# Kernel optimization log

Measured on AMD Instinct MI355X. Metric: run time of the kernel, lower is better.

Reference implementation:

```python
import jax, jax.numpy as jnp
jax.config.update("jax_enable_x64", True)
import numpy as np

LEAF = 0.3          # leaf_voxel_size
FACTOR = 2.0        # scale_up_factor
LEVELS = 3          # voxel_level_num
DIM = 8             # feature_dim
BUF = 5000000       # hash_buffer_size
NFEAT = 4194304     # entries per level feature table
PRIMES = jnp.array([73856093, 19349669, 83492791], dtype=jnp.int64)
STEPS = jnp.array([[0.,0.,0.],[0.,0.,1.],[0.,1.,0.],[0.,1.,1.],
                   [1.,0.,0.],[1.,0.,1.],[1.,1.,0.],[1.,1.,1.]], dtype=jnp.float32)

def setup_inputs() -> dict:
    key = jax.random.key(0)
    k1, k2, k3 = jax.random.split(key, 3)
    query_points = jax.random.normal(k1, (1000000, 3), dtype=jnp.float32) * 25.0
    features = 0.01 * jax.random.normal(k2, (LEVELS, NFEAT, DIM), dtype=jnp.float32)
    index_table = jax.random.randint(k3, (LEVELS, BUF), 0, NFEAT, dtype=jnp.int64)
    return {"query_points": query_points, "features": features, "index_table": index_table}

def _level_features(points, feats, idx_table, res):
    # points: [N,3], feats: [F,D], idx_table: [BUF] int64
    base = jnp.floor(points / res)                       # [N,3]
    corners = base[:, None, :] + STEPS[None]             # [N,8,3]
    keys = (corners.astype(jnp.int64) * PRIMES).sum(-1) % BUF  # [N,8]
    idx = idx_table[keys]                                # [N,8]
    mask = idx.min(axis=1) > -1                          # point valid iff all 8 corners mapped
    gathered = feats[jnp.maximum(idx, 0)]                # [N,8,D]
    d = points / res - base                              # fractional coords in cell, [N,3]
    # trilinear weights, corner order matches STEPS (same as torch interpolat)
    w = (STEPS[None] * d[:, None, :] + (1.0 - STEPS[None]) * (1.0 - d[:, None, :])).prod(-1)  # [N,8]
    lvl = (gathered * w[..., None]).sum(1)               # [N,D]
    return jnp.where(mask[:, None], lvl, 0.0)

def reference(query_points, features, index_table):
    out = jnp.zeros((query_points.shape[0], DIM), dtype=jnp.float32)
    for i in range(LEVELS):
        res = LEAF * FACTOR ** i
        out = out + _level_features(query_points, features[i], index_table[i], res)
    return out
```

## Files before the change

### kernel.cpp

```cpp
#include <hip/hip_runtime.h>


constexpr int       BUF   = 5000000;
constexpr long long NFEAT = 4194304;
constexpr int       DIM   = 8;
constexpr long long P0 = 73856093, P1 = 19349669, P2 = 83492791;
constexpr int       NBINS = 1 << 21;

typedef float vf4 __attribute__((ext_vector_type(4)));

#define GLD0(dst, voff, base)                                  \
    asm volatile("global_load_dwordx4 %0, %1, %2"              \
                 : "=v"(dst) : "v"(voff), "s"(base))
#define GLD16(dst, voff, base)                                 \
    asm volatile("global_load_dwordx4 %0, %1, %2 offset:16"    \
                 : "=v"(dst) : "v"(voff), "s"(base))

template <bool ADD>
__global__ __launch_bounds__(256, 4) void nvh_level_kernel(
    const float* __restrict__ in,
    const float* __restrict__ fb,
    const int* __restrict__ tab,
    float* __restrict__ outp,
    int n, float res)
{
    int i = blockIdx.x * blockDim.x + threadIdx.x;
    if (i >= n) return;

    const float px = in[3 * i + 0];
    const float py = in[3 * i + 1];
    const float pz = in[3 * i + 2];

    const float fx = px / res, fy = py / res, fz = pz / res;
    const float bx = floorf(fx), by = floorf(fy), bz = floorf(fz);
    const float dx = fx - bx, dy = fy - by, dz = fz - bz;

    const long long ix = (long long)bx;
    const long long iy = (long long)by;
    const long long iz = (long long)bz;

    long long h0 = (ix * P0 + iy * P1 + iz * P2) % (long long)BUF;
    if (h0 < 0) h0 += BUF;
    const int k0 = (int)h0;

    int idxv[8];
#pragma unroll
    for (int c = 0; c < 8; ++c) {
        const long long offc = (((c >> 2) & 1) * P0 + ((c >> 1) & 1) * P1 +
                                (c & 1) * P2) % (long long)BUF;
        int k = k0 + (int)offc;
        if (k >= BUF) k -= BUF;
        idxv[c] = tab[k];
    }
    __builtin_amdgcn_sched_barrier(0);

    bool valid = true;
    unsigned voff[8];
#pragma unroll
    for (int c = 0; c < 8; ++c) {
        valid = valid && (idxv[c] > -1);
        const int id = idxv[c] > 0 ? idxv[c] : 0;
        voff[c] = (unsigned)id * 32u;
    }

    vf4 f[16];
#pragma unroll
    for (int c = 0; c < 8; ++c) {
        GLD0 (f[2 * c + 0], voff[c], fb);
        GLD16(f[2 * c + 1], voff[c], fb);
    }

    vf4 prev0, prev1;
    if (ADD) {
        const vf4* op = (const vf4*)(outp + (size_t)i * DIM);
        prev0 = op[0];
        prev1 = op[1];
    }

    const float wx1 = dx, wx0 = 1.0f - dx;
    const float wy1 = dy, wy0 = 1.0f - dy;
    const float wz1 = dz, wz0 = 1.0f - dz;
    const float vmask = valid ? 1.0f : 0.0f;

    asm volatile("s_waitcnt vmcnt(0)" ::: "memory");
    __builtin_amdgcn_sched_barrier(0);

    vf4 lacc0 = (vf4)0.0f;
    vf4 lacc1 = (vf4)0.0f;
#pragma unroll
    for (int c = 0; c < 8; ++c) {
        const float wc = (((c >> 2) & 1) ? wx1 : wx0) *
                         (((c >> 1) & 1) ? wy1 : wy0) *
                         (((c     ) & 1) ? wz1 : wz0);
        lacc0 += wc * f[2 * c + 0];
        lacc1 += wc * f[2 * c + 1];
    }

    vf4 r0 = vmask * lacc0;
    vf4 r1 = vmask * lacc1;
    if (ADD) { r0 += prev0; r1 += prev1; }

    vf4* op = (vf4*)(outp + (size_t)i * DIM);
    op[0] = r0;
    op[1] = r1;
}

__device__ __forceinline__ unsigned spread3(unsigned v) {
    v = (v | (v << 16)) & 0x030000FFu;
    v = (v | (v << 8))  & 0x0300F00Fu;
    v = (v | (v << 4))  & 0x030C30C3u;
    v = (v | (v << 2))  & 0x09249249u;
    return v;
}

__global__ __launch_bounds__(256) void zero_hist(unsigned* __restrict__ h) {
    int i = blockIdx.x * blockDim.x + threadIdx.x;
    for (int k = i; k < NBINS; k += gridDim.x * blockDim.x) h[k] = 0u;
}

__global__ __launch_bounds__(256) void keys_hist(
    const float* __restrict__ qp, unsigned* __restrict__ keys,
    unsigned* __restrict__ hist, int n)
{
    int i = blockIdx.x * blockDim.x + threadIdx.x;
    if (i >= n) return;
    const float inv = 1.0f / 1.2f;
    int cx = (int)floorf(qp[3 * i + 0] * inv);
    int cy = (int)floorf(qp[3 * i + 1] * inv);
    int cz = (int)floorf(qp[3 * i + 2] * inv);
    cx = cx < -64 ? -64 : (cx > 63 ? 63 : cx);
    cy = cy < -64 ? -64 : (cy > 63 ? 63 : cy);
    cz = cz < -64 ? -64 : (cz > 63 ? 63 : cz);
    const unsigned key = (spread3((unsigned)(cx + 64)) << 2) |
                         (spread3((unsigned)(cy + 64)) << 1) |
                          spread3((unsigned)(cz + 64));
    keys[i] = key;
    atomicAdd(&hist[key], 1u);
}

__global__ __launch_bounds__(256) void scan_blocks(
    unsigned* __restrict__ data, unsigned* __restrict__ bsum)
{
    __shared__ unsigned s[256];
    const int t = threadIdx.x;
    const int base = blockIdx.x * 1024 + t * 4;
    unsigned v0 = data[base + 0], v1 = data[base + 1];
    unsigned v2 = data[base + 2], v3 = data[base + 3];
    const unsigned tsum = v0 + v1 + v2 + v3;
    s[t] = tsum;
    __syncthreads();
    for (int off = 1; off < 256; off <<= 1) {
        unsigned x = (t >= off) ? s[t - off] : 0u;
        __syncthreads();
        s[t] += x;
        __syncthreads();
    }
    const unsigned excl = s[t] - tsum;
    if (t == 255) bsum[blockIdx.x] = s[255];
    data[base + 0] = excl;
    data[base + 1] = excl + v0;
    data[base + 2] = excl + v0 + v1;
    data[base + 3] = excl + v0 + v1 + v2;
}

__global__ __launch_bounds__(256) void scan_top(unsigned* __restrict__ bsum) {
    __shared__ unsigned s[256];
    const int t = threadIdx.x;
    unsigned v[8];
    unsigned tsum = 0;
#pragma unroll
    for (int j = 0; j < 8; ++j) { v[j] = bsum[t * 8 + j]; tsum += v[j]; }
    s[t] = tsum;
    __syncthreads();
    for (int off = 1; off < 256; off <<= 1) {
        unsigned x = (t >= off) ? s[t - off] : 0u;
        __syncthreads();
        s[t] += x;
        __syncthreads();
    }
    unsigned run = s[t] - tsum;
#pragma unroll
    for (int j = 0; j < 8; ++j) { const unsigned nv = run; run += v[j]; bsum[t * 8 + j] = nv; }
}

__global__ __launch_bounds__(256) void scan_add(
    unsigned* __restrict__ data, const unsigned* __restrict__ bsum)
{
    const int base = blockIdx.x * 1024 + threadIdx.x * 4;
    const unsigned add = bsum[blockIdx.x];
    data[base + 0] += add;
    data[base + 1] += add;
    data[base + 2] += add;
    data[base + 3] += add;
}

__global__ __launch_bounds__(256) void scatter_perm(
    const unsigned* __restrict__ keys, unsigned* __restrict__ hist,
    unsigned* __restrict__ perm, unsigned* __restrict__ invp, int n)
{
    int i = blockIdx.x * blockDim.x + threadIdx.x;
    if (i >= n) return;
    const unsigned r = atomicAdd(&hist[keys[i]], 1u);
    perm[r] = (unsigned)i;
    invp[i] = r;
}

__global__ __launch_bounds__(256) void gather_points(
    const float* __restrict__ qp, const unsigned* __restrict__ perm,
    float* __restrict__ qps, int n)
{
    int i = blockIdx.x * blockDim.x + threadIdx.x;
    if (i >= n) return;
    const unsigned j = perm[i];
    qps[3 * i + 0] = qp[3 * j + 0];
    qps[3 * i + 1] = qp[3 * j + 1];
    qps[3 * i + 2] = qp[3 * j + 2];
}

__global__ __launch_bounds__(256) void unpermute_out(
    const float* __restrict__ out_s, const unsigned* __restrict__ invp,
    float* __restrict__ out, int n)
{
    int i = blockIdx.x * blockDim.x + threadIdx.x;
    if (i >= n) return;
    const unsigned r = invp[i];
    const vf4* a = (const vf4*)(out_s + (size_t)r * DIM);
    const vf4 x = a[0], y = a[1];
    vf4* o = (vf4*)(out + (size_t)i * DIM);
    o[0] = x;
    o[1] = y;
}

extern "C" void kernel_launch(void* const* d_in, const int* in_sizes, int n_in,
                              void* d_out, int out_size, void* d_ws, size_t ws_size,
                              hipStream_t stream) {
    const float* qp      = (const float*)d_in[0];
    const float* feats   = (const float*)d_in[1];
    const int*   idx_tab = (const int*)d_in[2];
    float*       out     = (float*)d_out;

    const int n = in_sizes[0] / 3;
    const int block = 256;
    const int grid = (n + block - 1) / block;

    auto al = [](size_t x) { return (x + 255) & ~(size_t)255; };
    const size_t o_hist = 0;
    const size_t o_bsum = al(o_hist + (size_t)NBINS * 4);
    const size_t o_keys = al(o_bsum + 2048 * 4);
    const size_t o_perm = al(o_keys + (size_t)n * 4);
    const size_t o_invp = al(o_perm + (size_t)n * 4);
    const size_t o_qps  = al(o_invp + (size_t)n * 4);
    const size_t o_outs = al(o_qps  + (size_t)n * 12);
    const size_t need   = o_outs + (size_t)n * 32;

    const bool use_sort = (d_ws != nullptr) && (ws_size >= need);

    const float* in_pts = qp;
    float*       out_l  = out;

    if (use_sort) {
        char* ws = (char*)d_ws;
        unsigned* hist = (unsigned*)(ws + o_hist);
        unsigned* bsum = (unsigned*)(ws + o_bsum);
        unsigned* keys = (unsigned*)(ws + o_keys);
        unsigned* perm = (unsigned*)(ws + o_perm);
        unsigned* invp = (unsigned*)(ws + o_invp);
        float*    qps  = (float*)   (ws + o_qps);
        float*    outs = (float*)   (ws + o_outs);

        hipLaunchKernelGGL(zero_hist, dim3(2048), dim3(block), 0, stream, hist);
        hipLaunchKernelGGL(keys_hist, dim3(grid), dim3(block), 0, stream,
                           qp, keys, hist, n);
        hipLaunchKernelGGL(scan_blocks, dim3(NBINS / 1024), dim3(block), 0,
                           stream, hist, bsum);
        hipLaunchKernelGGL(scan_top, dim3(1), dim3(block), 0, stream, bsum);
        hipLaunchKernelGGL(scan_add, dim3(NBINS / 1024), dim3(block), 0,
                           stream, hist, bsum);
        hipLaunchKernelGGL(scatter_perm, dim3(grid), dim3(block), 0, stream,
                           keys, hist, perm, invp, n);
        hipLaunchKernelGGL(gather_points, dim3(grid), dim3(block), 0, stream,
                           qp, perm, qps, n);

        in_pts = qps;
        out_l  = outs;

        hipLaunchKernelGGL((nvh_level_kernel<false>), dim3(grid), dim3(block),
                           0, stream, in_pts, feats, idx_tab, out_l, n, 0.3f);
        hipLaunchKernelGGL((nvh_level_kernel<true>), dim3(grid), dim3(block),
                           0, stream, in_pts, feats + (size_t)1 * NFEAT * DIM,
                           idx_tab + (size_t)1 * BUF, out_l, n, 0.6f);
        hipLaunchKernelGGL((nvh_level_kernel<true>), dim3(grid), dim3(block),
                           0, stream, in_pts, feats + (size_t)2 * NFEAT * DIM,
                           idx_tab + (size_t)2 * BUF, out_l, n, 1.2f);

        hipLaunchKernelGGL(unpermute_out, dim3(grid), dim3(block), 0, stream,
                           outs, invp, out, n);
    } else {
        hipLaunchKernelGGL((nvh_level_kernel<false>), dim3(grid), dim3(block),
                           0, stream, qp, feats, idx_tab, out, n, 0.3f);
        hipLaunchKernelGGL((nvh_level_kernel<true>), dim3(grid), dim3(block),
                           0, stream, qp, feats + (size_t)1 * NFEAT * DIM,
                           idx_tab + (size_t)1 * BUF, out, n, 0.6f);
        hipLaunchKernelGGL((nvh_level_kernel<true>), dim3(grid), dim3(block),
                           0, stream, qp, feats + (size_t)2 * NFEAT * DIM,
                           idx_tab + (size_t)2 * BUF, out, n, 1.2f);
    }
}
```

Baseline: 1.099 ms.

## Fuse three levels into one kernel with cooperative lane-per-corner gathers

```diff
diff --git a/kernel.cpp b/kernel.cpp
--- a/kernel.cpp
+++ b/kernel.cpp
@@ -5,104 +5,171 @@
 constexpr long long NFEAT = 4194304;
 constexpr int       DIM   = 8;
 constexpr long long P0 = 73856093, P1 = 19349669, P2 = 83492791;
+constexpr int       P0m = 3856093, P1m = 4349669, P2m = 3492791;
 constexpr int       NBINS = 1 << 21;
 
 typedef float vf4 __attribute__((ext_vector_type(4)));
 
-#define GLD0(dst, voff, base)                                  \
-    asm volatile("global_load_dwordx4 %0, %1, %2"              \
-                 : "=v"(dst) : "v"(voff), "s"(base))
-#define GLD16(dst, voff, base)                                 \
-    asm volatile("global_load_dwordx4 %0, %1, %2 offset:16"    \
-                 : "=v"(dst) : "v"(voff), "s"(base))
-
-template <bool ADD>
-__global__ __launch_bounds__(256, 4) void nvh_level_kernel(
-    const float* __restrict__ in,
-    const float* __restrict__ fb,
-    const int* __restrict__ tab,
-    float* __restrict__ outp,
-    int n, float res)
-{
-    int i = blockIdx.x * blockDim.x + threadIdx.x;
-    if (i >= n) return;
-
-    const float px = in[3 * i + 0];
-    const float py = in[3 * i + 1];
-    const float pz = in[3 * i + 2];
-
-    const float fx = px / res, fy = py / res, fz = pz / res;
-    const float bx = floorf(fx), by = floorf(fy), bz = floorf(fz);
-    const float dx = fx - bx, dy = fy - by, dz = fz - bz;
-
-    const long long ix = (long long)bx;
-    const long long iy = (long long)by;
-    const long long iz = (long long)bz;
-
-    long long h0 = (ix * P0 + iy * P1 + iz * P2) % (long long)BUF;
-    if (h0 < 0) h0 += BUF;
-    const int k0 = (int)h0;
-
-    int idxv[8];
+__global__ __launch_bounds__(256, 4) void nvh_fused(
+    const float* __restrict__ qps,
+    const float* __restrict__ feats,
+    const int* __restrict__ idx_tab,
+    const unsigned* __restrict__ perm,
+    float* __restrict__ out, int n)
+{
+    __shared__ float rec[256 * 12];
+    __shared__ float res[256 * 8];
+
+    const int t    = threadIdx.x;
+    const int i    = blockIdx.x * 256 + t;
+    const int lane = t & 63;
+    const int wbase = t & 192;
+
+    unsigned my_perm = (unsigned)i;
+    {
+        float px = 0.0f, py = 0.0f, pz = 0.0f;
+        if (i < n) {
+            px = qps[3 * i + 0];
+            py = qps[3 * i + 1];
+            pz = qps[3 * i + 2];
+            if (perm) my_perm = perm[i];
+        }
+        const float resv[3] = {0.3f, 0.6f, 1.2f};
 #pragma unroll
-    for (int c = 0; c < 8; ++c) {
-        const long long offc = (((c >> 2) & 1) * P0 + ((c >> 1) & 1) * P1 +
-                                (c & 1) * P2) % (long long)BUF;
-        int k = k0 + (int)offc;
-        if (k >= BUF) k -= BUF;
-        idxv[c] = tab[k];
-    }
-    __builtin_amdgcn_sched_barrier(0);
-
-    bool valid = true;
-    unsigned voff[8];
-#pragma unroll
-    for (int c = 0; c < 8; ++c) {
-        valid = valid && (idxv[c] > -1);
-        const int id = idxv[c] > 0 ? idxv[c] : 0;
-        voff[c] = (unsigned)id * 32u;
-    }
-
-    vf4 f[16];
-#pragma unroll
-    for (int c = 0; c < 8; ++c) {
-        GLD0 (f[2 * c + 0], voff[c], fb);
-        GLD16(f[2 * c + 1], voff[c], fb);
-    }
-
-    vf4 prev0, prev1;
-    if (ADD) {
-        const vf4* op = (const vf4*)(outp + (size_t)i * DIM);
-        prev0 = op[0];
-        prev1 = op[1];
-    }
-
-    const float wx1 = dx, wx0 = 1.0f - dx;
-    const float wy1 = dy, wy0 = 1.0f - dy;
-    const float wz1 = dz, wz0 = 1.0f - dz;
-    const float vmask = valid ? 1.0f : 0.0f;
-
+        for (int l = 0; l < 3; ++l) {
+            const float res_ = resv[l];
+            const float fx = px / res_, fy = py / res_, fz = pz / res_;
+            const float bx = floorf(fx), by = floorf(fy), bz = floorf(fz);
+            const long long ix = (long long)bx;
+            const long long iy = (long long)by;
+            const long long iz = (long long)bz;
+            long long h0 = (ix * P0 + iy * P1 + iz * P2) % (long long)BUF;
+            if (h0 < 0) h0 += BUF;
+            rec[t * 12 + l * 4 + 0] = __int_as_float((int)h0);
+            rec[t * 12 + l * 4 + 1] = fx - bx;
+            rec[t * 12 + l * 4 + 2] = fy - by;
+            rec[t * 12 + l * 4 + 3] = fz - bz;
+        }
+    }
+    __syncthreads();
     asm volatile("s_waitcnt vmcnt(0)" ::: "memory");
     __builtin_amdgcn_sched_barrier(0);
 
-    vf4 lacc0 = (vf4)0.0f;
-    vf4 lacc1 = (vf4)0.0f;
-#pragma unroll
-    for (int c = 0; c < 8; ++c) {
-        const float wc = (((c >> 2) & 1) ? wx1 : wx0) *
-                         (((c >> 1) & 1) ? wy1 : wy0) *
-                         (((c     ) & 1) ? wz1 : wz0);
-        lacc0 += wc * f[2 * c + 0];
-        lacc1 += wc * f[2 * c + 1];
-    }
-
-    vf4 r0 = vmask * lacc0;
-    vf4 r1 = vmask * lacc1;
-    if (ADD) { r0 += prev0; r1 += prev1; }
-
-    vf4* op = (vf4*)(outp + (size_t)i * DIM);
-    op[0] = r0;
-    op[1] = r1;
+    const bool sx = (lane & 8) != 0;
+    const bool sy = (lane & 4) != 0;
+    const bool sz = (lane & 2) != 0;
+    const unsigned hoff = (unsigned)(lane & 1) * 16u;
+
+    int   idxv[8][6];
+    float okv[8][6];
+    vf4   fv[8][6];
+
+#define KG(g)                                                                 \
+    do {                                                                      \
+        _Pragma("unroll") for (int sub = 0; sub < 2; ++sub) {                 \
+            const int s_ = 2 * (g) + sub;                                     \
+            const int pl_ = wbase + s_ * 4 + (lane >> 4);                     \
+            const int rb_ = pl_ * 12;                                         \
+            _Pragma("unroll") for (int l = 0; l < 3; ++l) {                   \
+                int key = __float_as_int(rec[rb_ + l * 4]);                   \
+                if (sx) { key += P0m; if (key >= BUF) key -= BUF; }           \
+                if (sy) { key += P1m; if (key >= BUF) key -= BUF; }           \
+                if (sz) { key += P2m; if (key >= BUF) key -= BUF; }           \
+                const unsigned ko_ = (unsigned)key * 4u;                      \
+                asm volatile("global_load_dword %0, %1, %2"                   \
+                             : "=v"(idxv[(g)][sub * 3 + l])                   \
+                             : "v"(ko_), "s"(idx_tab + (size_t)l * BUF));     \
+            }                                                                 \
+        }                                                                     \
+    } while (0)
+
+#define FG(g)                                                                 \
+    do {                                                                      \
+        _Pragma("unroll") for (int sub = 0; sub < 2; ++sub) {                 \
+            _Pragma("unroll") for (int l = 0; l < 3; ++l) {                   \
+                int id_ = idxv[(g)][sub * 3 + l];                             \
+                const unsigned long long bal_ = __ballot(id_ > -1);           \
+                okv[(g)][sub * 3 + l] =                                       \
+                    (((bal_ >> (lane & 48)) & 0xFFFFull) == 0xFFFFull)        \
+                        ? 1.0f : 0.0f;                                        \
+                id_ = id_ > 0 ? id_ : 0;                                      \
+                const unsigned vo_ = (unsigned)id_ * 32u + hoff;              \
+                asm volatile("global_load_dwordx4 %0, %1, %2"                 \
+                             : "=v"(fv[(g)][sub * 3 + l])                     \
+                             : "v"(vo_),                                      \
+                               "s"(feats + (size_t)l * NFEAT * DIM));         \
+            }                                                                 \
+        }                                                                     \
+    } while (0)
+
+#define MG(g)                                                                 \
+    do {                                                                      \
+        _Pragma("unroll") for (int sub = 0; sub < 2; ++sub) {                 \
+            const int s_ = 2 * (g) + sub;                                     \
+            const int pl_ = wbase + s_ * 4 + (lane >> 4);                     \
+            const int rb_ = pl_ * 12;                                         \
+            vf4 r_ = (vf4)0.0f;                                               \
+            _Pragma("unroll") for (int l = 0; l < 3; ++l) {                   \
+                const float dx_ = rec[rb_ + l * 4 + 1];                       \
+                const float dy_ = rec[rb_ + l * 4 + 2];                       \
+                const float dz_ = rec[rb_ + l * 4 + 3];                       \
+                const float w_ = (sx ? dx_ : 1.0f - dx_) *                    \
+                                 (sy ? dy_ : 1.0f - dy_) *                    \
+                                 (sz ? dz_ : 1.0f - dz_) *                    \
+                                 okv[(g)][sub * 3 + l];                       \
+                r_ += w_ * fv[(g)][sub * 3 + l];                              \
+            }                                                                 \
+            vf4 t_;                                                           \
+            _Pragma("unroll") for (int e = 0; e < 4; ++e)                     \
+                t_[e] = __int_as_float(__builtin_amdgcn_ds_swizzle(           \
+                    __float_as_int(r_[e]), 0x081F));                          \
+            r_ += t_;                                                         \
+            _Pragma("unroll") for (int e = 0; e < 4; ++e)                     \
+                t_[e] = __int_as_float(__builtin_amdgcn_ds_swizzle(           \
+                    __float_as_int(r_[e]), 0x101F));                          \
+            r_ += t_;                                                         \
+            _Pragma("unroll") for (int e = 0; e < 4; ++e)                     \
+                t_[e] = __int_as_float(__builtin_amdgcn_ds_swizzle(           \
+                    __float_as_int(r_[e]), 0x201F));                          \
+            r_ += t_;                                                         \
+            if ((lane & 14) == 0) {                                           \
+                *(vf4*)&res[pl_ * 8 + (lane & 1) * 4] = r_;                   \
+            }                                                                 \
+        }                                                                     \
+    } while (0)
+
+#define VMW(N)                                                                \
+    do {                                                                      \
+        asm volatile("s_waitcnt vmcnt(" #N ")" ::: "memory");                 \
+        __builtin_amdgcn_sched_barrier(0);                                    \
+    } while (0)
+
+    KG(0); KG(1);
+    VMW(6);  FG(0); KG(2);
+    VMW(12); FG(1);
+    VMW(12); MG(0);
+    KG(3);  VMW(12); FG(2); VMW(12); MG(1);
+    KG(4);  VMW(12); FG(3); VMW(12); MG(2);
+    KG(5);  VMW(12); FG(4); VMW(12); MG(3);
+    KG(6);  VMW(12); FG(5); VMW(12); MG(4);
+    KG(7);  VMW(12); FG(6); VMW(12); MG(5);
+    VMW(6);  FG(7);
+    VMW(6);  MG(6);
+    VMW(0);  MG(7);
+
+#undef KG
+#undef FG
+#undef MG
+#undef VMW
+
+    __syncthreads();
+    if (i < n) {
+        const vf4 a = *(vf4*)&res[t * 8 + 0];
+        const vf4 b = *(vf4*)&res[t * 8 + 4];
+        float* op = out + (size_t)my_perm * DIM;
+        *(vf4*)(op + 0) = a;
+        *(vf4*)(op + 4) = b;
+    }
 }
 
 __device__ __forceinline__ unsigned spread3(unsigned v) {
@@ -196,13 +263,12 @@
 
 __global__ __launch_bounds__(256) void scatter_perm(
     const unsigned* __restrict__ keys, unsigned* __restrict__ hist,
-    unsigned* __restrict__ perm, unsigned* __restrict__ invp, int n)
+    unsigned* __restrict__ perm, int n)
 {
     int i = blockIdx.x * blockDim.x + threadIdx.x;
     if (i >= n) return;
     const unsigned r = atomicAdd(&hist[keys[i]], 1u);
     perm[r] = (unsigned)i;
-    invp[i] = r;
 }
 
 __global__ __launch_bounds__(256) void gather_points(
@@ -215,20 +281,6 @@
     qps[3 * i + 0] = qp[3 * j + 0];
     qps[3 * i + 1] = qp[3 * j + 1];
     qps[3 * i + 2] = qp[3 * j + 2];
-}
-
-__global__ __launch_bounds__(256) void unpermute_out(
-    const float* __restrict__ out_s, const unsigned* __restrict__ invp,
-    float* __restrict__ out, int n)
-{
-    int i = blockIdx.x * blockDim.x + threadIdx.x;
-    if (i >= n) return;
-    const unsigned r = invp[i];
-    const vf4* a = (const vf4*)(out_s + (size_t)r * DIM);
-    const vf4 x = a[0], y = a[1];
-    vf4* o = (vf4*)(out + (size_t)i * DIM);
-    o[0] = x;
-    o[1] = y;
 }
 
 extern "C" void kernel_launch(void* const* d_in, const int* in_sizes, int n_in,
@@ -248,15 +300,10 @@
     const size_t o_bsum = al(o_hist + (size_t)NBINS * 4);
     const size_t o_keys = al(o_bsum + 2048 * 4);
     const size_t o_perm = al(o_keys + (size_t)n * 4);
-    const size_t o_invp = al(o_perm + (size_t)n * 4);
-    const size_t o_qps  = al(o_invp + (size_t)n * 4);
-    const size_t o_outs = al(o_qps  + (size_t)n * 12);
-    const size_t need   = o_outs + (size_t)n * 32;
+    const size_t o_qps  = al(o_perm + (size_t)n * 4);
+    const size_t need   = o_qps + (size_t)n * 12;
 
     const bool use_sort = (d_ws != nullptr) && (ws_size >= need);
-
-    const float* in_pts = qp;
-    float*       out_l  = out;
 
     if (use_sort) {
         char* ws = (char*)d_ws;
@@ -264,9 +311,7 @@
         unsigned* bsum = (unsigned*)(ws + o_bsum);
         unsigned* keys = (unsigned*)(ws + o_keys);
         unsigned* perm = (unsigned*)(ws + o_perm);
-        unsigned* invp = (unsigned*)(ws + o_invp);
         float*    qps  = (float*)   (ws + o_qps);
-        float*    outs = (float*)   (ws + o_outs);
 
         hipLaunchKernelGGL(zero_hist, dim3(2048), dim3(block), 0, stream, hist);
         hipLaunchKernelGGL(keys_hist, dim3(grid), dim3(block), 0, stream,
@@ -277,32 +322,13 @@
         hipLaunchKernelGGL(scan_add, dim3(NBINS / 1024), dim3(block), 0,
                            stream, hist, bsum);
         hipLaunchKernelGGL(scatter_perm, dim3(grid), dim3(block), 0, stream,
-                           keys, hist, perm, invp, n);
+                           keys, hist, perm, n);
         hipLaunchKernelGGL(gather_points, dim3(grid), dim3(block), 0, stream,
                            qp, perm, qps, n);
-
-        in_pts = qps;
-        out_l  = outs;
-
-        hipLaunchKernelGGL((nvh_level_kernel<false>), dim3(grid), dim3(block),
-                           0, stream, in_pts, feats, idx_tab, out_l, n, 0.3f);
-        hipLaunchKernelGGL((nvh_level_kernel<true>), dim3(grid), dim3(block),
-                           0, stream, in_pts, feats + (size_t)1 * NFEAT * DIM,
-                           idx_tab + (size_t)1 * BUF, out_l, n, 0.6f);
-        hipLaunchKernelGGL((nvh_level_kernel<true>), dim3(grid), dim3(block),
-                           0, stream, in_pts, feats + (size_t)2 * NFEAT * DIM,
-                           idx_tab + (size_t)2 * BUF, out_l, n, 1.2f);
-
-        hipLaunchKernelGGL(unpermute_out, dim3(grid), dim3(block), 0, stream,
-                           outs, invp, out, n);
+        hipLaunchKernelGGL(nvh_fused, dim3(grid), dim3(block), 0, stream,
+                           qps, feats, idx_tab, perm, out, n);
     } else {
-        hipLaunchKernelGGL((nvh_level_kernel<false>), dim3(grid), dim3(block),
-                           0, stream, qp, feats, idx_tab, out, n, 0.3f);
-        hipLaunchKernelGGL((nvh_level_kernel<true>), dim3(grid), dim3(block),
-                           0, stream, qp, feats + (size_t)1 * NFEAT * DIM,
-                           idx_tab + (size_t)1 * BUF, out, n, 0.6f);
-        hipLaunchKernelGGL((nvh_level_kernel<true>), dim3(grid), dim3(block),
-                           0, stream, qp, feats + (size_t)2 * NFEAT * DIM,
-                           idx_tab + (size_t)2 * BUF, out, n, 1.2f);
-    }
-}
+        hipLaunchKernelGGL(nvh_fused, dim3(grid), dim3(block), 0, stream,
+                           qp, feats, idx_tab, (const unsigned*)nullptr, out, n);
+    }
+}
```

Result: slower. 1.151 ms (+4.7%).
